# Optimization experiments

Hardware: AMD Instinct MI355X
Metric: run time of the kernel (lower is better)

## Reference

```python
import jax, jax.numpy as jnp
import numpy as np

B, T, D, H, DH, F, E, TOPK = 4, 1024, 1024, 16, 64, 4096, 8, 2
GATE_TEMP = 0.9
EPS = 1e-5


def _ln(x, g, b):
    m = jnp.mean(x, axis=-1, keepdims=True)
    v = jnp.mean((x - m) ** 2, axis=-1, keepdims=True)
    return (x - m) * jax.lax.rsqrt(v + EPS) * g + b


def setup_inputs() -> dict:
    key = jax.random.key(0)
    ks = jax.random.split(key, 16)
    s = 0.02
    inp = {
        'x': jax.random.normal(ks[0], (B, T, D), jnp.float32),
        'mask': jnp.tril(jnp.ones((1, 1, T, T), jnp.int32)),  # causal
        'ln1_g': jnp.ones((D,), jnp.float32), 'ln1_b': jnp.zeros((D,), jnp.float32),
        'wq': jax.random.normal(ks[1], (D, D), jnp.float32) * s, 'bq': jnp.zeros((D,), jnp.float32),
        'wk': jax.random.normal(ks[2], (D, D), jnp.float32) * s, 'bk': jnp.zeros((D,), jnp.float32),
        'wv': jax.random.normal(ks[3], (D, D), jnp.float32) * s, 'bv': jnp.zeros((D,), jnp.float32),
        'wo': jax.random.normal(ks[4], (D, D), jnp.float32) * s, 'bo': jnp.zeros((D,), jnp.float32),
        'ln2_g': jnp.ones((D,), jnp.float32), 'ln2_b': jnp.zeros((D,), jnp.float32),
        'gate_w': jax.random.normal(ks[5], (D, E), jnp.float32) * s, 'gate_b': jnp.zeros((E,), jnp.float32),
        'we1': jax.random.normal(ks[6], (E, D, F), jnp.float32) * s, 'be1': jnp.zeros((E, F), jnp.float32),
        'we2': jax.random.normal(ks[7], (E, F, D), jnp.float32) * s, 'be2': jnp.zeros((E, D), jnp.float32),
        'pn_g': jnp.ones((D,), jnp.float32), 'pn_b': jnp.zeros((D,), jnp.float32),
    }
    return inp


def reference(x, mask, ln1_g, ln1_b, wq, bq, wk, bk, wv, bv, wo, bo,
              ln2_g, ln2_b, gate_w, gate_b, we1, be1, we2, be2, pn_g, pn_b):
    # ---- attention branch (dropout = identity in eval) ----
    h = _ln(x, ln1_g, ln1_b)
    q = (h @ wq + bq).reshape(B, T, H, DH).transpose(0, 2, 1, 3)  # [B,H,T,DH]
    k = (h @ wk + bk).reshape(B, T, H, DH).transpose(0, 2, 1, 3)
    v = (h @ wv + bv).reshape(B, T, H, DH).transpose(0, 2, 1, 3)
    att = jnp.einsum('bhtd,bhsd->bhts', q, k) / jnp.sqrt(jnp.float32(DH))
    att = jnp.where(mask == 0, jnp.float32(-1e9), att)
    att = jax.nn.softmax(att, axis=-1)
    out = jnp.einsum('bhts,bhsd->bhtd', att, v).transpose(0, 2, 1, 3).reshape(B, T, D)
    x = x + (out @ wo + bo)

    # ---- MoE branch ----
    h = _ln(x, ln2_g, ln2_b)
    gate_logits = (h @ gate_w + gate_b) / GATE_TEMP        # [B,T,E]
    topk_vals, topk_idx = jax.lax.top_k(gate_logits, TOPK)
    keep = jnp.sum(jax.nn.one_hot(topk_idx, E, dtype=bool), axis=-2)  # [B,T,E] bool
    masked = jnp.where(keep, gate_logits, -jnp.inf)
    gate_probs = jax.nn.softmax(masked, axis=-1)            # [B,T,E]
    # dense all-expert FFN (exact GELU, dropout=identity)
    hid = jax.nn.gelu(jnp.einsum('btd,edf->btef', h, we1) + be1, approximate=False)
    expert_out = jnp.einsum('btef,efd->bted', hid, we2) + be2  # [B,T,E,D]
    moe = jnp.sum(gate_probs[..., None] * expert_out, axis=2)
    moe = _ln(moe, pn_g, pn_b)
    return x + moe
```

## Files before the change

kernel.cpp:

```cpp
#include <hip/hip_runtime.h>
#include <hip/hip_bf16.h>
#include <math.h>

#define B_ 4
#define T_ 1024
#define D_ 1024
#define H_ 16
#define DH_ 64
#define F_ 4096
#define E_ 8
#define NTOK 4096
#define EPS_ 1e-5f

typedef float f32x4 __attribute__((ext_vector_type(4)));
typedef __bf16 bf16x8 __attribute__((ext_vector_type(8)));
typedef _Float16 f16x8 __attribute__((ext_vector_type(8)));

__device__ __forceinline__ unsigned short f2bf(float f) {
    unsigned u = __float_as_uint(f);
    u = u + 0x7fffu + ((u >> 16) & 1u);
    return (unsigned short)(u >> 16);
}

__device__ __forceinline__ void splitf(float x, unsigned short& h, unsigned short& l) {
    _Float16 hf = (_Float16)x;
    _Float16 lf = (_Float16)((x - (float)hf) * 2048.0f);
    h = __builtin_bit_cast(unsigned short, hf);
    l = __builtin_bit_cast(unsigned short, lf);
}

__device__ __forceinline__ void blockreduce2(float& s, float& sq) {
    #pragma unroll
    for (int o = 32; o > 0; o >>= 1) { s += __shfl_xor(s, o); sq += __shfl_xor(sq, o); }
    __shared__ float ls[4], lq[4];
    int w = threadIdx.x >> 6;
    if ((threadIdx.x & 63) == 0) { ls[w] = s; lq[w] = sq; }
    __syncthreads();
    s = ls[0] + ls[1] + ls[2] + ls[3];
    sq = lq[0] + lq[1] + lq[2] + lq[3];
}

__global__ void k_zero(int* __restrict__ cnt) {
    if (threadIdx.x < E_) cnt[threadIdx.x] = 0;
}

__global__ void k_tconv(const float* __restrict__ in, unsigned short* __restrict__ out,
                        int R, int C) {
    __shared__ float tile[32][33];
    int e = blockIdx.z;
    const float* ine = in + (size_t)e * R * C;
    unsigned short* oute = out + (size_t)e * R * C;
    int tx = threadIdx.x & 31, ty = threadIdx.x >> 5;
    int c0 = blockIdx.x * 32, r0 = blockIdx.y * 32;
    #pragma unroll
    for (int j = 0; j < 32; j += 8)
        tile[ty + j][tx] = ine[(size_t)(r0 + ty + j) * C + c0 + tx];
    __syncthreads();
    #pragma unroll
    for (int j = 0; j < 32; j += 8)
        oute[(size_t)(c0 + ty + j) * R + r0 + tx] = f2bf(tile[tx][ty + j]);
}

__global__ void k_tconv_split(const float* __restrict__ w0, const float* __restrict__ w1,
        const float* __restrict__ w2, const float* __restrict__ w3,
        unsigned short* __restrict__ ohi, unsigned short* __restrict__ olo) {
    __shared__ float tile[32][33];
    int z = blockIdx.z;
    const float* in = (z == 0) ? w0 : ((z == 1) ? w1 : ((z == 2) ? w2 : w3));
    unsigned short* oh = ohi + (size_t)z * D_ * D_;
    unsigned short* ol = olo + (size_t)z * D_ * D_;
    int tx = threadIdx.x & 31, ty = threadIdx.x >> 5;
    int c0 = blockIdx.x * 32, r0 = blockIdx.y * 32;
    #pragma unroll
    for (int j = 0; j < 32; j += 8)
        tile[ty + j][tx] = in[(size_t)(r0 + ty + j) * D_ + c0 + tx];
    __syncthreads();
    #pragma unroll
    for (int j = 0; j < 32; j += 8) {
        unsigned short h, l;
        splitf(tile[tx][ty + j], h, l);
        size_t o = (size_t)(c0 + ty + j) * D_ + r0 + tx;
        oh[o] = h; ol[o] = l;
    }
}

__global__ void k_ln1(const float* __restrict__ x, const float* __restrict__ g,
                      const float* __restrict__ b, unsigned short* __restrict__ hh,
                      unsigned short* __restrict__ hl) {
    int row = blockIdx.x, t = threadIdx.x;
    f32x4 v = *(const f32x4*)(x + (size_t)row * D_ + t * 4);
    float s = v.x + v.y + v.z + v.w;
    float sq = v.x * v.x + v.y * v.y + v.z * v.z + v.w * v.w;
    blockreduce2(s, sq);
    float mean = s * (1.0f / D_);
    float var = sq * (1.0f / D_) - mean * mean;
    float inv = rsqrtf(var + EPS_);
    f32x4 gv = *(const f32x4*)(g + t * 4);
    f32x4 bv = *(const f32x4*)(b + t * 4);
    ushort4 oh, ol;
    float o0 = (v.x - mean) * inv * gv.x + bv.x;
    float o1 = (v.y - mean) * inv * gv.y + bv.y;
    float o2 = (v.z - mean) * inv * gv.z + bv.z;
    float o3 = (v.w - mean) * inv * gv.w + bv.w;
    splitf(o0, oh.x, ol.x); splitf(o1, oh.y, ol.y);
    splitf(o2, oh.z, ol.z); splitf(o3, oh.w, ol.w);
    *(ushort4*)(hh + (size_t)row * D_ + t * 4) = oh;
    *(ushort4*)(hl + (size_t)row * D_ + t * 4) = ol;
}

#define LDK2 40
__device__ __forceinline__ void mfma_split(const unsigned short* __restrict__ Ah,
        const unsigned short* __restrict__ Al, int strideA, int m0,
        const unsigned short* __restrict__ Bh, const unsigned short* __restrict__ Bl,
        int n0, int K, f32x4 acc1[4][4], f32x4 acc2[4][4]) {
    __shared__ unsigned short AsH[128 * LDK2];
    __shared__ unsigned short AsL[128 * LDK2];
    __shared__ unsigned short BsH[128 * LDK2];
    __shared__ unsigned short BsL[128 * LDK2];
    int t = threadIdx.x;
    int lane = t & 63, w = t >> 6;
    int wm = (w >> 1) * 64, wn = (w & 1) * 64;
    int r = t >> 1, kc = (t & 1) * 16;
    const unsigned short* pAh = Ah + (size_t)(m0 + r) * strideA + kc;
    const unsigned short* pAl = Al + (size_t)(m0 + r) * strideA + kc;
    const unsigned short* pBh = Bh + (size_t)(n0 + r) * K + kc;
    const unsigned short* pBl = Bl + (size_t)(n0 + r) * K + kc;
    int c15 = lane & 15, fk = (lane >> 4) * 8;
    unsigned short* wAh = &AsH[r * LDK2 + kc];
    unsigned short* wAl = &AsL[r * LDK2 + kc];
    unsigned short* wBh = &BsH[r * LDK2 + kc];
    unsigned short* wBl = &BsL[r * LDK2 + kc];
    uint4 ah0 = *(const uint4*)(pAh);
    uint4 ah1 = *(const uint4*)(pAh + 8);
    uint4 al0 = *(const uint4*)(pAl);
    uint4 al1 = *(const uint4*)(pAl + 8);
    uint4 bh0 = *(const uint4*)(pBh);
    uint4 bh1 = *(const uint4*)(pBh + 8);
    uint4 bl0 = *(const uint4*)(pBl);
    uint4 bl1 = *(const uint4*)(pBl + 8);
    for (int k0 = 0; k0 < K; k0 += 32) {
        __syncthreads();
        *(uint4*)(wAh) = ah0; *(uint4*)(wAh + 8) = ah1;
        *(uint4*)(wAl) = al0; *(uint4*)(wAl + 8) = al1;
        *(uint4*)(wBh) = bh0; *(uint4*)(wBh + 8) = bh1;
        *(uint4*)(wBl) = bl0; *(uint4*)(wBl + 8) = bl1;
        __syncthreads();
        if (k0 + 32 < K) {
            ah0 = *(const uint4*)(pAh + k0 + 32);
            ah1 = *(const uint4*)(pAh + k0 + 40);
            al0 = *(const uint4*)(pAl + k0 + 32);
            al1 = *(const uint4*)(pAl + k0 + 40);
            bh0 = *(const uint4*)(pBh + k0 + 32);
            bh1 = *(const uint4*)(pBh + k0 + 40);
            bl0 = *(const uint4*)(pBl + k0 + 32);
            bl1 = *(const uint4*)(pBl + k0 + 40);
        }
        f16x8 bfh[4], bfl[4];
        #pragma unroll
        for (int i = 0; i < 4; i++) {
            bfh[i] = *(const f16x8*)(&BsH[(wn + c15 + i * 16) * LDK2 + fk]);
            bfl[i] = *(const f16x8*)(&BsL[(wn + c15 + i * 16) * LDK2 + fk]);
        }
        #pragma unroll
        for (int mi = 0; mi < 4; mi++) {
            f16x8 afh = *(const f16x8*)(&AsH[(wm + c15 + mi * 16) * LDK2 + fk]);
            f16x8 afl = *(const f16x8*)(&AsL[(wm + c15 + mi * 16) * LDK2 + fk]);
            #pragma unroll
            for (int ni = 0; ni < 4; ni++) {
                acc1[mi][ni] = __builtin_amdgcn_mfma_f32_16x16x32_f16(afh, bfh[ni], acc1[mi][ni], 0, 0, 0);
                acc2[mi][ni] = __builtin_amdgcn_mfma_f32_16x16x32_f16(afh, bfl[ni], acc2[mi][ni], 0, 0, 0);
                acc2[mi][ni] = __builtin_amdgcn_mfma_f32_16x16x32_f16(afl, bfh[ni], acc2[mi][ni], 0, 0, 0);
            }
        }
    }
}

__global__ __launch_bounds__(256, 2) void k_qkv_split(
        const unsigned short* __restrict__ h1h, const unsigned short* __restrict__ h1l,
        const unsigned short* __restrict__ wth, const unsigned short* __restrict__ wtl,
        const float* __restrict__ bq, const float* __restrict__ bk, const float* __restrict__ bv,
        unsigned short* __restrict__ Qh, unsigned short* __restrict__ Ql,
        unsigned short* __restrict__ Kh, unsigned short* __restrict__ Kl,
        unsigned short* __restrict__ Vh, unsigned short* __restrict__ Vl) {
    int which = blockIdx.z;
    const unsigned short* Bh = wth + (size_t)which * D_ * D_;
    const unsigned short* Bl = wtl + (size_t)which * D_ * D_;
    const float* bias = (which == 0) ? bq : ((which == 1) ? bk : bv);
    unsigned short* Oh = (which == 0) ? Qh : ((which == 1) ? Kh : Vh);
    unsigned short* Ol = (which == 0) ? Ql : ((which == 1) ? Kl : Vl);
    f32x4 a1[4][4], a2[4][4];
    #pragma unroll
    for (int i = 0; i < 4; i++)
        #pragma unroll
        for (int j = 0; j < 4; j++) {
            a1[i][j].x = 0.f; a1[i][j].y = 0.f; a1[i][j].z = 0.f; a1[i][j].w = 0.f;
            a2[i][j].x = 0.f; a2[i][j].y = 0.f; a2[i][j].z = 0.f; a2[i][j].w = 0.f;
        }
    int m0 = blockIdx.y * 128, n0 = blockIdx.x * 128;
    mfma_split(h1h, h1l, D_, m0, Bh, Bl, n0, D_, a1, a2);
    int lane = threadIdx.x & 63, w = threadIdx.x >> 6;
    int wm = (w >> 1) * 64, wn = (w & 1) * 64;
    int c15 = lane & 15, quad = lane >> 4;
    #pragma unroll
    for (int mi = 0; mi < 4; mi++) {
        #pragma unroll
        for (int rr = 0; rr < 4; rr++) {
            int row = m0 + wm + mi * 16 + quad * 4 + rr;
            int bidx = row >> 10, tt = row & 1023;
            #pragma unroll
            for (int ni = 0; ni < 4; ni++) {
                int col = n0 + wn + ni * 16 + c15;
                float vv = a1[mi][ni][rr] + a2[mi][ni][rr] * (1.0f / 2048.0f) + bias[col];
                unsigned short hs, ls;
                splitf(vv, hs, ls);
                size_t idx = (((size_t)bidx * H_ + (col >> 6)) * T_ + tt) * DH_ + (col & 63);
                Oh[idx] = hs; Ol[idx] = ls;
            }
        }
    }
}

__global__ __launch_bounds__(256, 2) void k_proj_split(
        const unsigned short* __restrict__ ah, const unsigned short* __restrict__ al,
        const unsigned short* __restrict__ wh, const unsigned short* __restrict__ wl,
        const float* __restrict__ bo, const float* __restrict__ x, float* __restrict__ x2) {
    f32x4 a1[4][4], a2[4][4];
    #pragma unroll
    for (int i = 0; i < 4; i++)
        #pragma unroll
        for (int j = 0; j < 4; j++) {
            a1[i][j].x = 0.f; a1[i][j].y = 0.f; a1[i][j].z = 0.f; a1[i][j].w = 0.f;
            a2[i][j].x = 0.f; a2[i][j].y = 0.f; a2[i][j].z = 0.f; a2[i][j].w = 0.f;
        }
    int m0 = blockIdx.y * 128, n0 = blockIdx.x * 128;
    mfma_split(ah, al, D_, m0, wh, wl, n0, D_, a1, a2);
    int lane = threadIdx.x & 63, w = threadIdx.x >> 6;
    int wm = (w >> 1) * 64, wn = (w & 1) * 64;
    int c15 = lane & 15, quad = lane >> 4;
    #pragma unroll
    for (int mi = 0; mi < 4; mi++) {
        #pragma unroll
        for (int rr = 0; rr < 4; rr++) {
            int row = m0 + wm + mi * 16 + quad * 4 + rr;
            #pragma unroll
            for (int ni = 0; ni < 4; ni++) {
                int col = n0 + wn + ni * 16 + c15;
                float vv = a1[mi][ni][rr] + a2[mi][ni][rr] * (1.0f / 2048.0f) + bo[col]
                         + x[(size_t)row * D_ + col];
                x2[(size_t)row * D_ + col] = vv;
            }
        }
    }
}

#define NSLOT 40
__device__ __forceinline__ int slot_base(int qt) {
    const int base[16] = {0,1,2,3,4,6,8,10,12,15,18,21,24,28,32,36};
    return base[qt];
}
__device__ __forceinline__ int swzb(int r, int cb) {
    return r * 128 + (cb ^ ((r & 7) << 4));
}
__global__ __launch_bounds__(256, 2) void k_attn1(
        const unsigned short* __restrict__ Qh, const unsigned short* __restrict__ Ql,
        const unsigned short* __restrict__ Kh, const unsigned short* __restrict__ Kl,
        const unsigned short* __restrict__ Vh, const unsigned short* __restrict__ Vl,
        float* __restrict__ opart, float* __restrict__ mlpart) {
    __shared__ unsigned short QsH[64 * 64], QsL[64 * 64];
    __shared__ unsigned short KsH[64 * 64], KsL[64 * 64];
    __shared__ unsigned short VtH[64 * 64], VtL[64 * 64];
    __shared__ unsigned short PsH[64 * 64], PsL[64 * 64];
    int sp = blockIdx.x, qt = blockIdx.y, bh = blockIdx.z;
    int lim = (qt + 1) * 64;
    int s0 = sp * 256;
    if (s0 >= lim) return;
    int ntile = min(4, (lim - s0) >> 6);
    int t = threadIdx.x;
    int lane = t & 63, w = t >> 6;
    int c15 = lane & 15, quad = lane >> 4;
    size_t bho = (size_t)bh * T_ * DH_;
    {
        int q = t >> 2, cb = (t & 3) * 32;
        const unsigned short* sh = Qh + bho + (size_t)(qt * 64 + q) * DH_ + (cb >> 1);
        const unsigned short* sl = Ql + bho + (size_t)(qt * 64 + q) * DH_ + (cb >> 1);
        uint4 h0 = *(const uint4*)(sh);
        uint4 h1 = *(const uint4*)(sh + 8);
        uint4 l0 = *(const uint4*)(sl);
        uint4 l1 = *(const uint4*)(sl + 8);
        *(uint4*)((char*)QsH + swzb(q, cb))      = h0;
        *(uint4*)((char*)QsH + swzb(q, cb + 16)) = h1;
        *(uint4*)((char*)QsL + swzb(q, cb))      = l0;
        *(uint4*)((char*)QsL + swzb(q, cb + 16)) = l1;
    }
    f32x4 o1[4], o2[4];
    #pragma unroll
    for (int i = 0; i < 4; i++) {
        o1[i].x = 0.f; o1[i].y = 0.f; o1[i].z = 0.f; o1[i].w = 0.f;
        o2[i].x = 0.f; o2[i].y = 0.f; o2[i].z = 0.f; o2[i].w = 0.f;
    }
    float m[4] = {-1e30f, -1e30f, -1e30f, -1e30f};
    float l[4] = {0.f, 0.f, 0.f, 0.f};
    int qglob0 = qt * 64 + w * 16 + quad * 4;
    for (int kt = 0; kt < ntile; kt++) {
        int kbase = s0 + kt * 64;
        __syncthreads();
        {
            int r = t >> 2, cb = (t & 3) * 32;
            const unsigned short* sh = Kh + bho + (size_t)(kbase + r) * DH_ + (cb >> 1);
            const unsigned short* sl = Kl + bho + (size_t)(kbase + r) * DH_ + (cb >> 1);
            uint4 h0 = *(const uint4*)(sh);
            uint4 h1 = *(const uint4*)(sh + 8);
            uint4 l0 = *(const uint4*)(sl);
            uint4 l1 = *(const uint4*)(sl + 8);
            *(uint4*)((char*)KsH + swzb(r, cb))      = h0;
            *(uint4*)((char*)KsH + swzb(r, cb + 16)) = h1;
            *(uint4*)((char*)KsL + swzb(r, cb))      = l0;
            *(uint4*)((char*)KsL + swzb(r, cb + 16)) = l1;
        }
        {
            int k = t & 63, d0 = (t >> 6) * 16;
            const unsigned short* vh = Vh + bho + (size_t)(kbase + k) * DH_ + d0;
            const unsigned short* vl = Vl + bho + (size_t)(kbase + k) * DH_ + d0;
            unsigned short hv[16], lv[16];
            *(uint4*)(hv) = *(const uint4*)(vh);
            *(uint4*)(hv + 8) = *(const uint4*)(vh + 8);
            *(uint4*)(lv) = *(const uint4*)(vl);
            *(uint4*)(lv + 8) = *(const uint4*)(vl + 8);
            #pragma unroll
            for (int i = 0; i < 16; i++) {
                int d = d0 + i;
                *(unsigned short*)((char*)VtH + swzb(d, k * 2)) = hv[i];
                *(unsigned short*)((char*)VtL + swzb(d, k * 2)) = lv[i];
            }
        }
        __syncthreads();
        f32x4 s1[4], s2[4];
        #pragma unroll
        for (int i = 0; i < 4; i++) {
            s1[i].x = 0.f; s1[i].y = 0.f; s1[i].z = 0.f; s1[i].w = 0.f;
            s2[i].x = 0.f; s2[i].y = 0.f; s2[i].z = 0.f; s2[i].w = 0.f;
        }
        #pragma unroll
        for (int kk = 0; kk < 2; kk++) {
            int cb = kk * 64 + quad * 16;
            f16x8 ah = *(const f16x8*)((char*)QsH + swzb(w * 16 + c15, cb));
            f16x8 al = *(const f16x8*)((char*)QsL + swzb(w * 16 + c15, cb));
            #pragma unroll
            for (int ni = 0; ni < 4; ni++) {
                f16x8 bh16 = *(const f16x8*)((char*)KsH + swzb(ni * 16 + c15, cb));
                f16x8 bl16 = *(const f16x8*)((char*)KsL + swzb(ni * 16 + c15, cb));
                s1[ni] = __builtin_amdgcn_mfma_f32_16x16x32_f16(ah, bh16, s1[ni], 0, 0, 0);
                s2[ni] = __builtin_amdgcn_mfma_f32_16x16x32_f16(ah, bl16, s2[ni], 0, 0, 0);
                s2[ni] = __builtin_amdgcn_mfma_f32_16x16x32_f16(al, bh16, s2[ni], 0, 0, 0);
            }
        }
        f32x4 p[4];
        #pragma unroll
        for (int ni = 0; ni < 4; ni++)
            p[ni] = s1[ni] * 0.125f + s2[ni] * 6.103515625e-5f;
        #pragma unroll
        for (int ni = 0; ni < 4; ni++) {
            int kglob = kbase + c15 + 16 * ni;
            #pragma unroll
            for (int r = 0; r < 4; r++)
                p[ni][r] = (kglob <= qglob0 + r) ? p[ni][r] : -1e30f;
        }
        float alpha[4];
        #pragma unroll
        for (int r = 0; r < 4; r++) {
            float rm = fmaxf(fmaxf(p[0][r], p[1][r]), fmaxf(p[2][r], p[3][r]));
            rm = fmaxf(rm, __shfl_xor(rm, 1));
            rm = fmaxf(rm, __shfl_xor(rm, 2));
            rm = fmaxf(rm, __shfl_xor(rm, 4));
            rm = fmaxf(rm, __shfl_xor(rm, 8));
            float mnew = fmaxf(m[r], rm);
            alpha[r] = __expf(m[r] - mnew);
            m[r] = mnew;
            float rs = 0.f;
            #pragma unroll
            for (int ni = 0; ni < 4; ni++) {
                float pv = (p[ni][r] > -1e29f) ? __expf(p[ni][r] - mnew) : 0.f;
                p[ni][r] = pv;
                rs += pv;
            }
            rs += __shfl_xor(rs, 1);
            rs += __shfl_xor(rs, 2);
            rs += __shfl_xor(rs, 4);
            rs += __shfl_xor(rs, 8);
            l[r] = l[r] * alpha[r] + rs;
        }
        #pragma unroll
        for (int ni = 0; ni < 4; ni++) {
            o1[ni].x *= alpha[0]; o1[ni].y *= alpha[1]; o1[ni].z *= alpha[2]; o1[ni].w *= alpha[3];
            o2[ni].x *= alpha[0]; o2[ni].y *= alpha[1]; o2[ni].z *= alpha[2]; o2[ni].w *= alpha[3];
        }
        #pragma unroll
        for (int ni = 0; ni < 4; ni++) {
            int cbyte = (c15 + 16 * ni) * 2;
            #pragma unroll
            for (int r = 0; r < 4; r++) {
                unsigned short hs, ls;
                splitf(p[ni][r], hs, ls);
                int row = w * 16 + quad * 4 + r;
                *(unsigned short*)((char*)PsH + swzb(row, cbyte)) = hs;
                *(unsigned short*)((char*)PsL + swzb(row, cbyte)) = ls;
            }
        }
        __syncthreads();
        #pragma unroll
        for (int kk = 0; kk < 2; kk++) {
            int cb = kk * 64 + quad * 16;
            f16x8 ph = *(const f16x8*)((char*)PsH + swzb(w * 16 + c15, cb));
            f16x8 pl = *(const f16x8*)((char*)PsL + swzb(w * 16 + c15, cb));
            #pragma unroll
            for (int ni = 0; ni < 4; ni++) {
                f16x8 vh16 = *(const f16x8*)((char*)VtH + swzb(ni * 16 + c15, cb));
                f16x8 vl16 = *(const f16x8*)((char*)VtL + swzb(ni * 16 + c15, cb));
                o1[ni] = __builtin_amdgcn_mfma_f32_16x16x32_f16(ph, vh16, o1[ni], 0, 0, 0);
                o2[ni] = __builtin_amdgcn_mfma_f32_16x16x32_f16(ph, vl16, o2[ni], 0, 0, 0);
                o2[ni] = __builtin_amdgcn_mfma_f32_16x16x32_f16(pl, vh16, o2[ni], 0, 0, 0);
            }
        }
    }
    int slot = bh * NSLOT + slot_base(qt) + sp;
    float* dst = opart + (size_t)slot * 64 * 64;
    #pragma unroll
    for (int ni = 0; ni < 4; ni++) {
        #pragma unroll
        for (int r = 0; r < 4; r++) {
            float val = o1[ni][r] + o2[ni][r] * (1.0f / 2048.0f);
            dst[(size_t)(w * 16 + quad * 4 + r) * 64 + c15 + 16 * ni] = val;
        }
    }
    if (c15 == 0) {
        #pragma unroll
        for (int r = 0; r < 4; r++) {
            int row = w * 16 + quad * 4 + r;
            mlpart[slot * 128 + row * 2 + 0] = m[r];
            mlpart[slot * 128 + row * 2 + 1] = l[r];
        }
    }
}

__global__ void k_attn2(const float* __restrict__ opart, const float* __restrict__ mlpart,
                        unsigned short* __restrict__ atth, unsigned short* __restrict__ attl) {
    int qt = blockIdx.x, bh = blockIdx.y;
    int b = bh >> 4, h = bh & 15;
    int nsp = (qt >> 2) + 1;
    int slot0 = bh * NSLOT + slot_base(qt);
    int tid = threadIdx.x;
    int q = tid >> 2, d0 = (tid & 3) * 16;
    float ms[4], ls[4];
    float mx = -1e30f;
    for (int s = 0; s < nsp; s++) {
        ms[s] = mlpart[(slot0 + s) * 128 + q * 2 + 0];
        ls[s] = mlpart[(slot0 + s) * 128 + q * 2 + 1];
        mx = fmaxf(mx, ms[s]);
    }
    float den = 0.f;
    f32x4 num[4];
    #pragma unroll
    for (int i = 0; i < 4; i++) { num[i].x = 0.f; num[i].y = 0.f; num[i].z = 0.f; num[i].w = 0.f; }
    for (int s = 0; s < nsp; s++) {
        float sc = __expf(ms[s] - mx);
        den += ls[s] * sc;
        const float* src = opart + ((size_t)(slot0 + s) * 64 + q) * 64 + d0;
        #pragma unroll
        for (int i = 0; i < 4; i++) num[i] += sc * *(const f32x4*)(src + i * 4);
    }
    float inv = 1.0f / den;
    size_t base = ((size_t)(b * T_ + qt * 64 + q)) * D_ + h * DH_ + d0;
    #pragma unroll
    for (int i = 0; i < 4; i++) {
        f32x4 v = num[i] * inv;
        ushort4 hh, ll;
        splitf(v.x, hh.x, ll.x); splitf(v.y, hh.y, ll.y);
        splitf(v.z, hh.z, ll.z); splitf(v.w, hh.w, ll.w);
        *(ushort4*)(atth + base + i * 4) = hh;
        *(ushort4*)(attl + base + i * 4) = ll;
    }
}

__global__ void k_ln2_gate(const float* __restrict__ x2, const float* __restrict__ g,
        const float* __restrict__ bb, const float* __restrict__ gw, const float* __restrict__ gb,
        unsigned short* __restrict__ h2, int* __restrict__ cnt, int* __restrict__ lst,
        int* __restrict__ te, int* __restrict__ ts, float* __restrict__ tp) {
    int row = blockIdx.x, t = threadIdx.x;
    f32x4 v = *(const f32x4*)(x2 + (size_t)row * D_ + t * 4);
    float s = v.x + v.y + v.z + v.w;
    float sq = v.x * v.x + v.y * v.y + v.z * v.z + v.w * v.w;
    blockreduce2(s, sq);
    float mean = s * (1.0f / D_), var = sq * (1.0f / D_) - mean * mean;
    float inv = rsqrtf(var + EPS_);
    f32x4 gv = *(const f32x4*)(g + t * 4);
    f32x4 bv = *(const f32x4*)(bb + t * 4);
    float hv[4];
    #pragma unroll
    for (int i = 0; i < 4; i++) hv[i] = (v[i] - mean) * inv * gv[i] + bv[i];
    ushort4 hb;
    hb.x = f2bf(hv[0]); hb.y = f2bf(hv[1]); hb.z = f2bf(hv[2]); hb.w = f2bf(hv[3]);
    *(ushort4*)(&h2[(size_t)row * D_ + t * 4]) = hb;
    float lg[8];
    #pragma unroll
    for (int e2 = 0; e2 < 8; e2++) lg[e2] = 0.f;
    #pragma unroll
    for (int i = 0; i < 4; i++) {
        const float* gr = gw + (size_t)(t * 4 + i) * E_;
        f32x4 g0 = *(const f32x4*)(gr);
        f32x4 g1 = *(const f32x4*)(gr + 4);
        lg[0] = fmaf(hv[i], g0.x, lg[0]); lg[1] = fmaf(hv[i], g0.y, lg[1]);
        lg[2] = fmaf(hv[i], g0.z, lg[2]); lg[3] = fmaf(hv[i], g0.w, lg[3]);
        lg[4] = fmaf(hv[i], g1.x, lg[4]); lg[5] = fmaf(hv[i], g1.y, lg[5]);
        lg[6] = fmaf(hv[i], g1.z, lg[6]); lg[7] = fmaf(hv[i], g1.w, lg[7]);
    }
    #pragma unroll
    for (int o = 32; o > 0; o >>= 1) {
        #pragma unroll
        for (int e2 = 0; e2 < 8; e2++) lg[e2] += __shfl_xor(lg[e2], o);
    }
    __shared__ float lred[4][8];
    int w = t >> 6;
    if ((t & 63) == 0) {
        #pragma unroll
        for (int e2 = 0; e2 < 8; e2++) lred[w][e2] = lg[e2];
    }
    __syncthreads();
    if (t == 0) {
        float L[8];
        #pragma unroll
        for (int e2 = 0; e2 < 8; e2++)
            L[e2] = (lred[0][e2] + lred[1][e2] + lred[2][e2] + lred[3][e2] + gb[e2]) / 0.9f;
        int e0 = 0, e1 = -1; float v0 = L[0], v1 = -3e38f;
        #pragma unroll
        for (int e2 = 1; e2 < 8; e2++) {
            float xv = L[e2];
            if (xv > v0)      { v1 = v0; e1 = e0; v0 = xv; e0 = e2; }
            else if (xv > v1) { v1 = xv; e1 = e2; }
        }
        float ex = __expf(v1 - v0);
        float denom = 1.0f + ex;
        float p0 = 1.0f / denom, p1 = ex / denom;
        int s0 = atomicAdd(&cnt[e0], 1);
        int s1 = atomicAdd(&cnt[e1], 1);
        lst[e0 * NTOK + s0] = row;
        lst[e1 * NTOK + s1] = row;
        te[row * 2 + 0] = e0; te[row * 2 + 1] = e1;
        ts[row * 2 + 0] = s0; ts[row * 2 + 1] = s1;
        tp[row * 2 + 0] = p0; tp[row * 2 + 1] = p1;
    }
}

__global__ void k_offs(const int* __restrict__ cnt, int* __restrict__ offs) {
    if (threadIdx.x == 0 && blockIdx.x == 0) {
        int a = 0;
        #pragma unroll
        for (int e = 0; e < E_; e++) { offs[e] = a; a += cnt[e]; }
    }
}

#define LDK 40
__device__ __forceinline__ void mfma_core(const unsigned short* __restrict__ A, int strideA,
        const int* __restrict__ gather, int m0, int M,
        const unsigned short* __restrict__ Bt, int n0, int K, f32x4 acc[4][4]) {
    __shared__ unsigned short As[128 * LDK];
    __shared__ unsigned short Bs[128 * LDK];
    int t = threadIdx.x;
    int lane = t & 63, w = t >> 6;
    int wm = (w >> 1) * 64, wn = (w & 1) * 64;
    int r = t >> 1, kc = (t & 1) * 16;
    int arow;
    if (gather) { int mm = m0 + r; arow = gather[mm < M ? mm : 0]; }
    else arow = m0 + r;
    const unsigned short* Ap = A + (size_t)arow * strideA + kc;
    const unsigned short* Bp = Bt + (size_t)(n0 + r) * K + kc;
    int c15 = lane & 15, fk = (lane >> 4) * 8;
    unsigned short* AsW = &As[r * LDK + kc];
    unsigned short* BsW = &Bs[r * LDK + kc];
    uint4 a0 = *(const uint4*)(Ap);
    uint4 a1 = *(const uint4*)(Ap + 8);
    uint4 b0 = *(const uint4*)(Bp);
    uint4 b1 = *(const uint4*)(Bp + 8);
    for (int k0 = 0; k0 < K; k0 += 32) {
        __syncthreads();
        *(uint4*)(AsW) = a0; *(uint4*)(AsW + 8) = a1;
        *(uint4*)(BsW) = b0; *(uint4*)(BsW + 8) = b1;
        __syncthreads();
        if (k0 + 32 < K) {
            a0 = *(const uint4*)(Ap + k0 + 32);
            a1 = *(const uint4*)(Ap + k0 + 40);
            b0 = *(const uint4*)(Bp + k0 + 32);
            b1 = *(const uint4*)(Bp + k0 + 40);
        }
        bf16x8 af[4], bfr[4];
        #pragma unroll
        for (int i = 0; i < 4; i++) {
            af[i]  = *(const bf16x8*)(&As[(wm + c15 + i * 16) * LDK + fk]);
            bfr[i] = *(const bf16x8*)(&Bs[(wn + c15 + i * 16) * LDK + fk]);
        }
        #pragma unroll
        for (int mi = 0; mi < 4; mi++)
            #pragma unroll
            for (int ni = 0; ni < 4; ni++)
                acc[mi][ni] = __builtin_amdgcn_mfma_f32_16x16x32_bf16(af[mi], bfr[ni], acc[mi][ni], 0, 0, 0);
    }
}

__global__ __launch_bounds__(256, 2) void k_moe1(const unsigned short* __restrict__ h2,
        const unsigned short* __restrict__ w1t, const float* __restrict__ be1,
        const int* __restrict__ cnt, const int* __restrict__ offs, const int* __restrict__ lst,
        unsigned short* __restrict__ hid) {
    int e = blockIdx.z;
    int M = cnt[e];
    int m0 = blockIdx.y * 128;
    if (m0 >= M) return;
    int n0 = blockIdx.x * 128;
    f32x4 acc[4][4];
    #pragma unroll
    for (int i = 0; i < 4; i++)
        #pragma unroll
        for (int j = 0; j < 4; j++) { acc[i][j].x = 0.f; acc[i][j].y = 0.f; acc[i][j].z = 0.f; acc[i][j].w = 0.f; }
    mfma_core(h2, D_, lst + e * NTOK, m0, M, w1t + (size_t)e * F_ * D_, n0, D_, acc);
    int lane = threadIdx.x & 63, w = threadIdx.x >> 6;
    int wm = (w >> 1) * 64, wn = (w & 1) * 64;
    int base = offs[e];
    const float* b1 = be1 + (size_t)e * F_;
    int c15 = lane & 15, quad = lane >> 4;
    #pragma unroll
    for (int mi = 0; mi < 4; mi++) {
        #pragma unroll
        for (int rr = 0; rr < 4; rr++) {
            int row = m0 + wm + mi * 16 + quad * 4 + rr;
            if (row < M) {
                size_t rb = (size_t)(base + row) * F_;
                #pragma unroll
                for (int ni = 0; ni < 4; ni++) {
                    int col = n0 + wn + ni * 16 + c15;
                    float xv = acc[mi][ni][rr] + b1[col];
                    float ge = 0.5f * xv * (1.0f + erff(xv * 0.70710678118654752f));
                    hid[rb + col] = f2bf(ge);
                }
            }
        }
    }
}

__global__ __launch_bounds__(256, 2) void k_moe2(const unsigned short* __restrict__ hid,
        const unsigned short* __restrict__ w2t, const float* __restrict__ be2,
        const int* __restrict__ cnt, const int* __restrict__ offs, float* __restrict__ eo) {
    int e = blockIdx.z;
    int M = cnt[e];
    int m0 = blockIdx.y * 128;
    if (m0 >= M) return;
    int n0 = blockIdx.x * 128;
    int base = offs[e];
    f32x4 acc[4][4];
    #pragma unroll
    for (int i = 0; i < 4; i++)
        #pragma unroll
        for (int j = 0; j < 4; j++) { acc[i][j].x = 0.f; acc[i][j].y = 0.f; acc[i][j].z = 0.f; acc[i][j].w = 0.f; }
    mfma_core(hid + (size_t)base * F_, F_, nullptr, m0, M, w2t + (size_t)e * D_ * F_, n0, F_, acc);
    int lane = threadIdx.x & 63, w = threadIdx.x >> 6;
    int wm = (w >> 1) * 64, wn = (w & 1) * 64;
    const float* b2 = be2 + (size_t)e * D_;
    int c15 = lane & 15, quad = lane >> 4;
    #pragma unroll
    for (int mi = 0; mi < 4; mi++) {
        #pragma unroll
        for (int rr = 0; rr < 4; rr++) {
            int row = m0 + wm + mi * 16 + quad * 4 + rr;
            if (row < M) {
                size_t rb = (size_t)(base + row) * D_;
                #pragma unroll
                for (int ni = 0; ni < 4; ni++) {
                    int col = n0 + wn + ni * 16 + c15;
                    eo[rb + col] = acc[mi][ni][rr] + b2[col];
                }
            }
        }
    }
}

__global__ void k_final(const float* __restrict__ x2, const float* __restrict__ eo,
        const int* __restrict__ te, const int* __restrict__ ts, const float* __restrict__ tp,
        const int* __restrict__ offs, const float* __restrict__ png, const float* __restrict__ pnb,
        float* __restrict__ out) {
    int row = blockIdx.x, t = threadIdx.x;
    int e0 = te[row * 2], e1 = te[row * 2 + 1];
    size_t g0 = (size_t)(offs[e0] + ts[row * 2]);
    size_t g1 = (size_t)(offs[e1] + ts[row * 2 + 1]);
    float p0 = tp[row * 2], p1 = tp[row * 2 + 1];
    f32x4 a = *(const f32x4*)(eo + g0 * D_ + t * 4);
    f32x4 b = *(const f32x4*)(eo + g1 * D_ + t * 4);
    f32x4 mo = p0 * a + p1 * b;
    float s = mo.x + mo.y + mo.z + mo.w;
    float sq = mo.x * mo.x + mo.y * mo.y + mo.z * mo.z + mo.w * mo.w;
    blockreduce2(s, sq);
    float mean = s * (1.0f / D_), var = sq * (1.0f / D_) - mean * mean;
    float inv = rsqrtf(var + EPS_);
    f32x4 gv = *(const f32x4*)(png + t * 4);
    f32x4 bv = *(const f32x4*)(pnb + t * 4);
    f32x4 xv = *(const f32x4*)(x2 + (size_t)row * D_ + t * 4);
    f32x4 o;
    o.x = xv.x + (mo.x - mean) * inv * gv.x + bv.x;
    o.y = xv.y + (mo.y - mean) * inv * gv.y + bv.y;
    o.z = xv.z + (mo.z - mean) * inv * gv.z + bv.z;
    o.w = xv.w + (mo.w - mean) * inv * gv.w + bv.w;
    *(f32x4*)(out + (size_t)row * D_ + t * 4) = o;
}

extern "C" void kernel_launch(void* const* d_in, const int* in_sizes, int n_in,
                              void* d_out, int out_size, void* d_ws, size_t ws_size,
                              hipStream_t stream) {
    (void)in_sizes; (void)n_in; (void)out_size; (void)ws_size;
    const float* x    = (const float*)d_in[0];
    const float* ln1g = (const float*)d_in[2];
    const float* ln1b = (const float*)d_in[3];
    const float* wq   = (const float*)d_in[4];
    const float* bq   = (const float*)d_in[5];
    const float* wk   = (const float*)d_in[6];
    const float* bk   = (const float*)d_in[7];
    const float* wv   = (const float*)d_in[8];
    const float* bv   = (const float*)d_in[9];
    const float* wo   = (const float*)d_in[10];
    const float* bo   = (const float*)d_in[11];
    const float* ln2g = (const float*)d_in[12];
    const float* ln2b = (const float*)d_in[13];
    const float* gw   = (const float*)d_in[14];
    const float* gb   = (const float*)d_in[15];
    const float* we1  = (const float*)d_in[16];
    const float* be1  = (const float*)d_in[17];
    const float* we2  = (const float*)d_in[18];
    const float* be2  = (const float*)d_in[19];
    const float* png  = (const float*)d_in[20];
    const float* pnb  = (const float*)d_in[21];
    float* out = (float*)d_out;

    char* ws = (char*)d_ws;
    size_t off = 0;
    auto alloc = [&](size_t bytes) { void* p = ws + off; off += (bytes + 255) & ~(size_t)255; return p; };
    unsigned short* h1h = (unsigned short*)alloc((size_t)NTOK * D_ * 2);
    unsigned short* h1l = (unsigned short*)alloc((size_t)NTOK * D_ * 2);
    unsigned short* Qhp = (unsigned short*)alloc((size_t)NTOK * D_ * 2);
    unsigned short* Qlp = (unsigned short*)alloc((size_t)NTOK * D_ * 2);
    unsigned short* Khp = (unsigned short*)alloc((size_t)NTOK * D_ * 2);
    unsigned short* Klp = (unsigned short*)alloc((size_t)NTOK * D_ * 2);
    unsigned short* Vhp = (unsigned short*)alloc((size_t)NTOK * D_ * 2);
    unsigned short* Vlp = (unsigned short*)alloc((size_t)NTOK * D_ * 2);
    unsigned short* atth = (unsigned short*)alloc((size_t)NTOK * D_ * 2);
    unsigned short* attl = (unsigned short*)alloc((size_t)NTOK * D_ * 2);
    float* x2  = (float*)alloc((size_t)NTOK * D_ * 4);
    unsigned short* h2  = (unsigned short*)alloc((size_t)NTOK * D_ * 2);
    unsigned short* w1t = (unsigned short*)alloc((size_t)E_ * D_ * F_ * 2);
    unsigned short* w2t = (unsigned short*)alloc((size_t)E_ * D_ * F_ * 2);
    unsigned short* hid = (unsigned short*)alloc((size_t)(2 * NTOK + 128) * F_ * 2);
    float* eo  = (float*)alloc((size_t)(2 * NTOK) * D_ * 4);
    float* opart = (float*)alloc((size_t)64 * NSLOT * 64 * 64 * 4);
    float* mlpart= (float*)alloc((size_t)64 * NSLOT * 128 * 4);
    unsigned short* wsh = (unsigned short*)alloc((size_t)4 * D_ * D_ * 2);
    unsigned short* wsl = (unsigned short*)alloc((size_t)4 * D_ * D_ * 2);
    int* cnt   = (int*)alloc(256);
    int* offs  = (int*)alloc(256);
    int* lst   = (int*)alloc((size_t)E_ * NTOK * 4);
    int* te    = (int*)alloc((size_t)NTOK * 2 * 4);
    int* ts    = (int*)alloc((size_t)NTOK * 2 * 4);
    float* tp  = (float*)alloc((size_t)NTOK * 2 * 4);

    k_zero<<<dim3(1), dim3(64), 0, stream>>>(cnt);
    k_tconv<<<dim3(F_ / 32, D_ / 32, E_), dim3(256), 0, stream>>>(we1, w1t, D_, F_);
    k_tconv<<<dim3(D_ / 32, F_ / 32, E_), dim3(256), 0, stream>>>(we2, w2t, F_, D_);
    k_tconv_split<<<dim3(D_ / 32, D_ / 32, 4), dim3(256), 0, stream>>>(wq, wk, wv, wo, wsh, wsl);
    k_ln1<<<dim3(NTOK), dim3(256), 0, stream>>>(x, ln1g, ln1b, h1h, h1l);
    k_qkv_split<<<dim3(D_ / 128, NTOK / 128, 3), dim3(256), 0, stream>>>(
        h1h, h1l, wsh, wsl, bq, bk, bv, Qhp, Qlp, Khp, Klp, Vhp, Vlp);
    k_attn1<<<dim3(4, T_ / 64, B_ * H_), dim3(256), 0, stream>>>(
        Qhp, Qlp, Khp, Klp, Vhp, Vlp, opart, mlpart);
    k_attn2<<<dim3(T_ / 64, B_ * H_), dim3(256), 0, stream>>>(opart, mlpart, atth, attl);
    k_proj_split<<<dim3(D_ / 128, NTOK / 128, 1), dim3(256), 0, stream>>>(
        atth, attl, wsh + (size_t)3 * D_ * D_, wsl + (size_t)3 * D_ * D_, bo, x, x2);
    k_ln2_gate<<<dim3(NTOK), dim3(256), 0, stream>>>(x2, ln2g, ln2b, gw, gb, h2, cnt, lst, te, ts, tp);
    k_offs<<<dim3(1), dim3(64), 0, stream>>>(cnt, offs);
    k_moe1<<<dim3(F_ / 128, NTOK / 128, E_), dim3(256), 0, stream>>>(h2, w1t, be1, cnt, offs, lst, hid);
    k_moe2<<<dim3(D_ / 128, NTOK / 128, E_), dim3(256), 0, stream>>>(hid, w2t, be2, cnt, offs, eo);
    k_final<<<dim3(NTOK), dim3(256), 0, stream>>>(x2, eo, te, ts, tp, offs, png, pnb, out);
}
```

Baseline: 1.078 ms.

## Split K dimension in output projection and expert down-projection GEMMs

The attention output projection and the MoE second GEMM now each split K in two, with each half launched as a separate grid z-slice writing fp32 partial sums. The partials are summed, together with the biases and residual, in the following elementwise kernels (ln2_gate and final). The goal is more blocks and better CU occupancy on the mi355x for GEMMs whose tile grid is small or uneven per expert. The cost is extra global traffic for the partial buffers, which reuse the opart and h1h workspace regions.

```diff
diff --git a/kernel.cpp b/kernel.cpp
--- a/kernel.cpp
+++ b/kernel.cpp
@@ -112,7 +112,7 @@
 __device__ __forceinline__ void mfma_split(const unsigned short* __restrict__ Ah,
         const unsigned short* __restrict__ Al, int strideA, int m0,
         const unsigned short* __restrict__ Bh, const unsigned short* __restrict__ Bl,
-        int n0, int K, f32x4 acc1[4][4], f32x4 acc2[4][4]) {
+        int strideB, int n0, int K, f32x4 acc1[4][4], f32x4 acc2[4][4]) {
     __shared__ unsigned short AsH[128 * LDK2];
     __shared__ unsigned short AsL[128 * LDK2];
     __shared__ unsigned short BsH[128 * LDK2];
@@ -123,8 +123,8 @@
     int r = t >> 1, kc = (t & 1) * 16;
     const unsigned short* pAh = Ah + (size_t)(m0 + r) * strideA + kc;
     const unsigned short* pAl = Al + (size_t)(m0 + r) * strideA + kc;
-    const unsigned short* pBh = Bh + (size_t)(n0 + r) * K + kc;
-    const unsigned short* pBl = Bl + (size_t)(n0 + r) * K + kc;
+    const unsigned short* pBh = Bh + (size_t)(n0 + r) * strideB + kc;
+    const unsigned short* pBl = Bl + (size_t)(n0 + r) * strideB + kc;
     int c15 = lane & 15, fk = (lane >> 4) * 8;
     unsigned short* wAh = &AsH[r * LDK2 + kc];
     unsigned short* wAl = &AsL[r * LDK2 + kc];
@@ -197,7 +197,7 @@
             a2[i][j].x = 0.f; a2[i][j].y = 0.f; a2[i][j].z = 0.f; a2[i][j].w = 0.f;
         }
     int m0 = blockIdx.y * 128, n0 = blockIdx.x * 128;
-    mfma_split(h1h, h1l, D_, m0, Bh, Bl, n0, D_, a1, a2);
+    mfma_split(h1h, h1l, D_, m0, Bh, Bl, D_, n0, D_, a1, a2);
     int lane = threadIdx.x & 63, w = threadIdx.x >> 6;
     int wm = (w >> 1) * 64, wn = (w & 1) * 64;
     int c15 = lane & 15, quad = lane >> 4;
@@ -223,7 +223,8 @@
 __global__ __launch_bounds__(256, 2) void k_proj_split(
         const unsigned short* __restrict__ ah, const unsigned short* __restrict__ al,
         const unsigned short* __restrict__ wh, const unsigned short* __restrict__ wl,
-        const float* __restrict__ bo, const float* __restrict__ x, float* __restrict__ x2) {
+        float* __restrict__ xp) {
+    int ks = blockIdx.z;
     f32x4 a1[4][4], a2[4][4];
     #pragma unroll
     for (int i = 0; i < 4; i++)
@@ -233,7 +234,9 @@
             a2[i][j].x = 0.f; a2[i][j].y = 0.f; a2[i][j].z = 0.f; a2[i][j].w = 0.f;
         }
     int m0 = blockIdx.y * 128, n0 = blockIdx.x * 128;
-    mfma_split(ah, al, D_, m0, wh, wl, n0, D_, a1, a2);
+    mfma_split(ah + ks * 512, al + ks * 512, D_, m0,
+               wh + ks * 512, wl + ks * 512, D_, n0, 512, a1, a2);
+    float* dst = xp + (size_t)ks * NTOK * D_;
     int lane = threadIdx.x & 63, w = threadIdx.x >> 6;
     int wm = (w >> 1) * 64, wn = (w & 1) * 64;
     int c15 = lane & 15, quad = lane >> 4;
@@ -245,9 +248,7 @@
             #pragma unroll
             for (int ni = 0; ni < 4; ni++) {
                 int col = n0 + wn + ni * 16 + c15;
-                float vv = a1[mi][ni][rr] + a2[mi][ni][rr] * (1.0f / 2048.0f) + bo[col]
-                         + x[(size_t)row * D_ + col];
-                x2[(size_t)row * D_ + col] = vv;
+                dst[(size_t)row * D_ + col] = a1[mi][ni][rr] + a2[mi][ni][rr] * (1.0f / 2048.0f);
             }
         }
     }
@@ -481,12 +482,18 @@
     }
 }
 
-__global__ void k_ln2_gate(const float* __restrict__ x2, const float* __restrict__ g,
-        const float* __restrict__ bb, const float* __restrict__ gw, const float* __restrict__ gb,
+__global__ void k_ln2_gate(const float* __restrict__ xp, const float* __restrict__ bo,
+        const float* __restrict__ xin, float* __restrict__ x2,
+        const float* __restrict__ g, const float* __restrict__ bb,
+        const float* __restrict__ gw, const float* __restrict__ gb,
         unsigned short* __restrict__ h2, int* __restrict__ cnt, int* __restrict__ lst,
         int* __restrict__ te, int* __restrict__ ts, float* __restrict__ tp) {
     int row = blockIdx.x, t = threadIdx.x;
-    f32x4 v = *(const f32x4*)(x2 + (size_t)row * D_ + t * 4);
+    f32x4 v = *(const f32x4*)(xp + (size_t)row * D_ + t * 4)
+            + *(const f32x4*)(xp + (size_t)NTOK * D_ + (size_t)row * D_ + t * 4)
+            + *(const f32x4*)(bo + t * 4)
+            + *(const f32x4*)(xin + (size_t)row * D_ + t * 4);
+    *(f32x4*)(x2 + (size_t)row * D_ + t * 4) = v;
     float s = v.x + v.y + v.z + v.w;
     float sq = v.x * v.x + v.y * v.y + v.z * v.z + v.w * v.w;
     blockreduce2(s, sq);
@@ -561,7 +568,7 @@
 #define LDK 40
 __device__ __forceinline__ void mfma_core(const unsigned short* __restrict__ A, int strideA,
         const int* __restrict__ gather, int m0, int M,
-        const unsigned short* __restrict__ Bt, int n0, int K, f32x4 acc[4][4]) {
+        const unsigned short* __restrict__ Bt, int strideB, int n0, int K, f32x4 acc[4][4]) {
     __shared__ unsigned short As[128 * LDK];
     __shared__ unsigned short Bs[128 * LDK];
     int t = threadIdx.x;
@@ -572,7 +579,7 @@
     if (gather) { int mm = m0 + r; arow = gather[mm < M ? mm : 0]; }
     else arow = m0 + r;
     const unsigned short* Ap = A + (size_t)arow * strideA + kc;
-    const unsigned short* Bp = Bt + (size_t)(n0 + r) * K + kc;
+    const unsigned short* Bp = Bt + (size_t)(n0 + r) * strideB + kc;
     int c15 = lane & 15, fk = (lane >> 4) * 8;
     unsigned short* AsW = &As[r * LDK + kc];
     unsigned short* BsW = &Bs[r * LDK + kc];
@@ -619,7 +626,7 @@
     for (int i = 0; i < 4; i++)
         #pragma unroll
         for (int j = 0; j < 4; j++) { acc[i][j].x = 0.f; acc[i][j].y = 0.f; acc[i][j].z = 0.f; acc[i][j].w = 0.f; }
-    mfma_core(h2, D_, lst + e * NTOK, m0, M, w1t + (size_t)e * F_ * D_, n0, D_, acc);
+    mfma_core(h2, D_, lst + e * NTOK, m0, M, w1t + (size_t)e * F_ * D_, D_, n0, D_, acc);
     int lane = threadIdx.x & 63, w = threadIdx.x >> 6;
     int wm = (w >> 1) * 64, wn = (w & 1) * 64;
     int base = offs[e];
@@ -645,9 +652,10 @@
 }
 
 __global__ __launch_bounds__(256, 2) void k_moe2(const unsigned short* __restrict__ hid,
-        const unsigned short* __restrict__ w2t, const float* __restrict__ be2,
-        const int* __restrict__ cnt, const int* __restrict__ offs, float* __restrict__ eo) {
-    int e = blockIdx.z;
+        const unsigned short* __restrict__ w2t,
+        const int* __restrict__ cnt, const int* __restrict__ offs, float* __restrict__ eop) {
+    int ez = blockIdx.z;
+    int e = ez >> 1, ks = ez & 1;
     int M = cnt[e];
     int m0 = blockIdx.y * 128;
     if (m0 >= M) return;
@@ -658,10 +666,11 @@
     for (int i = 0; i < 4; i++)
         #pragma unroll
         for (int j = 0; j < 4; j++) { acc[i][j].x = 0.f; acc[i][j].y = 0.f; acc[i][j].z = 0.f; acc[i][j].w = 0.f; }
-    mfma_core(hid + (size_t)base * F_, F_, nullptr, m0, M, w2t + (size_t)e * D_ * F_, n0, F_, acc);
+    mfma_core(hid + (size_t)base * F_ + ks * (F_ / 2), F_, nullptr, m0, M,
+              w2t + (size_t)e * D_ * F_ + ks * (F_ / 2), F_, n0, F_ / 2, acc);
+    float* dst = eop + (size_t)ks * 2 * NTOK * D_ + (size_t)base * D_;
     int lane = threadIdx.x & 63, w = threadIdx.x >> 6;
     int wm = (w >> 1) * 64, wn = (w & 1) * 64;
-    const float* b2 = be2 + (size_t)e * D_;
     int c15 = lane & 15, quad = lane >> 4;
     #pragma unroll
     for (int mi = 0; mi < 4; mi++) {
@@ -669,18 +678,18 @@
         for (int rr = 0; rr < 4; rr++) {
             int row = m0 + wm + mi * 16 + quad * 4 + rr;
             if (row < M) {
-                size_t rb = (size_t)(base + row) * D_;
                 #pragma unroll
                 for (int ni = 0; ni < 4; ni++) {
                     int col = n0 + wn + ni * 16 + c15;
-                    eo[rb + col] = acc[mi][ni][rr] + b2[col];
+                    dst[(size_t)row * D_ + col] = acc[mi][ni][rr];
                 }
             }
         }
     }
 }
 
-__global__ void k_final(const float* __restrict__ x2, const float* __restrict__ eo,
+__global__ void k_final(const float* __restrict__ x2, const float* __restrict__ eop,
+        const float* __restrict__ be2,
         const int* __restrict__ te, const int* __restrict__ ts, const float* __restrict__ tp,
         const int* __restrict__ offs, const float* __restrict__ png, const float* __restrict__ pnb,
         float* __restrict__ out) {
@@ -689,8 +698,13 @@
     size_t g0 = (size_t)(offs[e0] + ts[row * 2]);
     size_t g1 = (size_t)(offs[e1] + ts[row * 2 + 1]);
     float p0 = tp[row * 2], p1 = tp[row * 2 + 1];
-    f32x4 a = *(const f32x4*)(eo + g0 * D_ + t * 4);
-    f32x4 b = *(const f32x4*)(eo + g1 * D_ + t * 4);
+    const size_t HALF = (size_t)2 * NTOK * D_;
+    f32x4 a = *(const f32x4*)(eop + g0 * D_ + t * 4)
+            + *(const f32x4*)(eop + HALF + g0 * D_ + t * 4)
+            + *(const f32x4*)(be2 + (size_t)e0 * D_ + t * 4);
+    f32x4 b = *(const f32x4*)(eop + g1 * D_ + t * 4)
+            + *(const f32x4*)(eop + HALF + g1 * D_ + t * 4)
+            + *(const f32x4*)(be2 + (size_t)e1 * D_ + t * 4);
     f32x4 mo = p0 * a + p1 * b;
     float s = mo.x + mo.y + mo.z + mo.w;
     float sq = mo.x * mo.x + mo.y * mo.y + mo.z * mo.z + mo.w * mo.w;
@@ -753,7 +767,6 @@
     unsigned short* w1t = (unsigned short*)alloc((size_t)E_ * D_ * F_ * 2);
     unsigned short* w2t = (unsigned short*)alloc((size_t)E_ * D_ * F_ * 2);
     unsigned short* hid = (unsigned short*)alloc((size_t)(2 * NTOK + 128) * F_ * 2);
-    float* eo  = (float*)alloc((size_t)(2 * NTOK) * D_ * 4);
     float* opart = (float*)alloc((size_t)64 * NSLOT * 64 * 64 * 4);
     float* mlpart= (float*)alloc((size_t)64 * NSLOT * 128 * 4);
     unsigned short* wsh = (unsigned short*)alloc((size_t)4 * D_ * D_ * 2);
@@ -764,6 +777,8 @@
     int* te    = (int*)alloc((size_t)NTOK * 2 * 4);
     int* ts    = (int*)alloc((size_t)NTOK * 2 * 4);
     float* tp  = (float*)alloc((size_t)NTOK * 2 * 4);
+    float* xp  = opart;
+    float* eop = (float*)h1h;
 
     k_zero<<<dim3(1), dim3(64), 0, stream>>>(cnt);
     k_tconv<<<dim3(F_ / 32, D_ / 32, E_), dim3(256), 0, stream>>>(we1, w1t, D_, F_);
@@ -775,11 +790,12 @@
     k_attn1<<<dim3(4, T_ / 64, B_ * H_), dim3(256), 0, stream>>>(
         Qhp, Qlp, Khp, Klp, Vhp, Vlp, opart, mlpart);
     k_attn2<<<dim3(T_ / 64, B_ * H_), dim3(256), 0, stream>>>(opart, mlpart, atth, attl);
-    k_proj_split<<<dim3(D_ / 128, NTOK / 128, 1), dim3(256), 0, stream>>>(
-        atth, attl, wsh + (size_t)3 * D_ * D_, wsl + (size_t)3 * D_ * D_, bo, x, x2);
-    k_ln2_gate<<<dim3(NTOK), dim3(256), 0, stream>>>(x2, ln2g, ln2b, gw, gb, h2, cnt, lst, te, ts, tp);
+    k_proj_split<<<dim3(D_ / 128, NTOK / 128, 2), dim3(256), 0, stream>>>(
+        atth, attl, wsh + (size_t)3 * D_ * D_, wsl + (size_t)3 * D_ * D_, xp);
+    k_ln2_gate<<<dim3(NTOK), dim3(256), 0, stream>>>(
+        xp, bo, x, x2, ln2g, ln2b, gw, gb, h2, cnt, lst, te, ts, tp);
     k_offs<<<dim3(1), dim3(64), 0, stream>>>(cnt, offs);
     k_moe1<<<dim3(F_ / 128, NTOK / 128, E_), dim3(256), 0, stream>>>(h2, w1t, be1, cnt, offs, lst, hid);
-    k_moe2<<<dim3(D_ / 128, NTOK / 128, E_), dim3(256), 0, stream>>>(hid, w2t, be2, cnt, offs, eo);
-    k_final<<<dim3(NTOK), dim3(256), 0, stream>>>(x2, eo, te, ts, tp, offs, png, pnb, out);
-}
+    k_moe2<<<dim3(D_ / 128, NTOK / 128, E_ * 2), dim3(256), 0, stream>>>(hid, w2t, cnt, offs, eop);
+    k_final<<<dim3(NTOK), dim3(256), 0, stream>>>(x2, eop, be2, te, ts, tp, offs, png, pnb, out);
+}
```

Measured after the change: 1.022 ms. 1.05x faster.
